# Kernel tuning notes

Measured on AMD Instinct MI355X. Metric: run time of the kernel, lower is better.

## Reference

```python
import jax, jax.numpy as jnp
import numpy as np

B, T, META = 2, 1024, 6
VOCAB, MVOCAB = 32000, 1000
D, H, L = 512, 8, 6
HS = D // H          # 64
T1 = T + META        # 1030
CHUNK = 6            # sliding/chunk granularity hard-coded in generate_matrix
LN_EPS = 1e-5


def _layernorm(x, g, b):
    mu = jnp.mean(x, axis=-1, keepdims=True)
    var = jnp.mean((x - mu) ** 2, axis=-1, keepdims=True)
    return (x - mu) * jax.lax.rsqrt(var + LN_EPS) * g + b


def _pos_encoding(t, d):
    # torch: sin((position // 6) * div_term), cos(...) interleaved even/odd
    pos = jnp.floor(jnp.arange(t, dtype=jnp.float32) / CHUNK)
    div = jnp.exp(jnp.arange(0, d, 2, dtype=jnp.float32) * (-np.log(10000.0) / d))
    ang = pos[:, None] * div[None, :]                     # [t, d/2]
    enc = jnp.zeros((t, d), dtype=jnp.float32)
    enc = enc.at[:, 0::2].set(jnp.sin(ang))
    enc = enc.at[:, 1::2].set(jnp.cos(ang))
    return enc


def _mask(n):
    # row i attends to cols [0, (i//6+1)*6) plus the last 6 (metadata) cols
    r = jnp.arange(n)
    return (r[None, :] < (r[:, None] // CHUNK + 1) * CHUNK) | (r[None, :] >= n - CHUNK)


def setup_inputs() -> dict:
    key = jax.random.key(0)
    ks = jax.random.split(key, 16)
    s = 0.02
    n = lambda k, shp: jax.random.normal(k, shp, dtype=jnp.float32) * s
    return {
        "idx": jax.random.randint(ks[0], (B, T), 0, VOCAB),
        "metadata_idx": jax.random.randint(ks[1], (B, META), 0, MVOCAB),
        "tok_emb": n(ks[2], (VOCAB, D)),
        "meta_emb": n(ks[3], (MVOCAB, D)),
        "Wq": n(ks[4], (L, H, D, HS)),
        "Wk": n(ks[5], (L, H, D, HS)),
        "Wv": n(ks[6], (L, H, D, HS)),
        "Wo": n(ks[7], (L, D, D)),
        "bo": jnp.zeros((L, D), jnp.float32),
        "W1": n(ks[8], (L, D, 4 * D)),
        "b1": jnp.zeros((L, 4 * D), jnp.float32),
        "W2": n(ks[9], (L, 4 * D, D)),
        "b2": jnp.zeros((L, D), jnp.float32),
        "ln1_g": jnp.ones((L, D), jnp.float32),
        "ln1_b": jnp.zeros((L, D), jnp.float32),
        "ln2_g": jnp.ones((L, D), jnp.float32),
        "ln2_b": jnp.zeros((L, D), jnp.float32),
        "lnf_g": jnp.ones((D,), jnp.float32),
        "lnf_b": jnp.zeros((D,), jnp.float32),
        "Wlm": n(ks[10], (D, VOCAB)),
        "blm": jnp.zeros((VOCAB,), jnp.float32),
    }


def reference(idx, metadata_idx, tok_emb, meta_emb, Wq, Wk, Wv, Wo, bo,
              W1, b1, W2, b2, ln1_g, ln1_b, ln2_g, ln2_b, lnf_g, lnf_b, Wlm, blm):
    x = tok_emb[idx] + _pos_encoding(T, D)                 # [B, T, D]
    x = jnp.concatenate([x, meta_emb[metadata_idx]], axis=1)  # [B, T1, D]
    scale = D ** -0.5          # NOTE: original scales by full n_embd, not head_size
    mask = _mask(T1)
    neg_inf = jnp.float32(-jnp.inf)
    for l in range(L):
        h = _layernorm(x, ln1_g[l], ln1_b[l])
        q = jnp.einsum('btd,hde->bhte', h, Wq[l])          # [B, H, T1, HS]
        k = jnp.einsum('btd,hde->bhte', h, Wk[l])
        v = jnp.einsum('btd,hde->bhte', h, Wv[l])
        wei = jnp.einsum('bhqe,bhke->bhqk', q, k) * scale  # [B, H, T1, T1]
        wei = jnp.where(mask, wei, neg_inf)
        wei = jax.nn.softmax(wei, axis=-1)
        o = jnp.einsum('bhqk,bhke->bhqe', wei, v)          # [B, H, T1, HS]
        o = jnp.transpose(o, (0, 2, 1, 3)).reshape(x.shape[0], T1, D)
        x = x + o @ Wo[l] + bo[l]
        h = _layernorm(x, ln2_g[l], ln2_b[l])
        x = x + jax.nn.relu(h @ W1[l] + b1[l]) @ W2[l] + b2[l]
    x = _layernorm(x, lnf_g, lnf_b)
    logits = x @ Wlm + blm                                  # [B, T1, VOCAB]
    return logits[:, :T, :]
```

## Files before the change

kernel.cpp:

```cpp
#include <hip/hip_runtime.h>
#include <hip/hip_bf16.h>
#include <math.h>

#define TT     1024
#define METAN  6
#define TT1    1030
#define BB     2
#define DD     512
#define HH     8
#define HSZ    64
#define LL     6
#define NVOCAB 32000
#define MROWS  2060
#define MPAD   2176
#define SCALE  0.044194173824159216f

typedef float  f32x4  __attribute__((ext_vector_type(4)));
typedef __bf16 bf16x8 __attribute__((ext_vector_type(8)));

__device__ __forceinline__ __bf16 f2bf(float f) { return (__bf16)f; }

__device__ __forceinline__ void glds16(const __bf16* g, const __bf16* l) {
  __builtin_amdgcn_global_load_lds(
      (const __attribute__((address_space(1))) unsigned int*)g,
      (__attribute__((address_space(3))) unsigned int*)l, 16, 0, 0);
}

__device__ __forceinline__ bf16x8 ln8v(float4 v0, float4 v1, float mu, float rs,
                                       float4 g0, float4 g1, float4 b0, float4 b1) {
  float vv[8] = {v0.x, v0.y, v0.z, v0.w, v1.x, v1.y, v1.z, v1.w};
  float gg[8] = {g0.x, g0.y, g0.z, g0.w, g1.x, g1.y, g1.z, g1.w};
  float bb[8] = {b0.x, b0.y, b0.z, b0.w, b1.x, b1.y, b1.z, b1.w};
  bf16x8 r;
#pragma unroll
  for (int j = 0; j < 8; j++) r[j] = f2bf((vv[j] - mu) * rs * gg[j] + bb[j]);
  return r;
}
__device__ __forceinline__ bf16x8 ln8(const float* xp, float mu, float rs,
                                      const float* g, const float* b) {
  return ln8v(*(const float4*)xp, *(const float4*)(xp + 4), mu, rs,
              *(const float4*)g, *(const float4*)(g + 4),
              *(const float4*)b, *(const float4*)(b + 4));
}

__global__ void k_embedw(const int* idx, const int* midx, const float* tok,
                         const float* met, float* x, float* ps, float* pq)
{
  const int sub = threadIdx.x >> 7;
  const int tl  = threadIdx.x & 127;
  const int d0  = tl * 4;
  int row = blockIdx.x * 2 + sub;
  int b = row / TT1, tk = row - b * TT1;
  float v[4];
  if (tk < TT) {
    const float* e = tok + (size_t)idx[b * TT + tk] * DD;
    float pos = (float)(tk / 6);
#pragma unroll
    for (int j = 0; j < 4; j += 2) {
      int i = (d0 + j) >> 1;
      float dv = expf((float)i * (-2.0f * 9.210340371976184f / 512.0f));
      float ang = pos * dv;
      v[j]     = e[d0 + j]     + sinf(ang);
      v[j + 1] = e[d0 + j + 1] + cosf(ang);
    }
  } else {
    const float* e = met + (size_t)midx[b * METAN + (tk - TT)] * DD;
#pragma unroll
    for (int j = 0; j < 4; j++) v[j] = e[d0 + j];
  }
  *(float4*)&x[(size_t)row * DD + d0] = *(float4*)v;
  float s = v[0] + v[1] + v[2] + v[3];
  float q = v[0]*v[0] + v[1]*v[1] + v[2]*v[2] + v[3]*v[3];
#pragma unroll
  for (int msk = 1; msk < 16; msk <<= 1) { s += __shfl_xor(s, msk); q += __shfl_xor(q, msk); }
  if ((tl & 15) == 0) {
    ps[(size_t)row * 8 + (tl >> 4)] = s;
    pq[(size_t)row * 8 + (tl >> 4)] = q;
  }
}

__global__ void k_lnpw(const float* x, const float* ps, const float* pq,
                       const float* g, const float* b, __bf16* xf)
{
  const int sub = threadIdx.x >> 6;
  const int lane = threadIdx.x & 63;
  int row = blockIdx.x * 4 + sub;
  int sr = (row >> 10) * TT1 + (row & 1023);
  float s = 0.f, q = 0.f;
#pragma unroll
  for (int j = 0; j < 8; j++) { s += ps[(size_t)sr * 8 + j]; q += pq[(size_t)sr * 8 + j]; }
  float mu = s * (1.0f / 512.0f);
  float rs = rsqrtf(fmaxf(q * (1.0f / 512.0f) - mu * mu, 0.f) + 1e-5f);
  bf16x8 o = ln8(&x[(size_t)sr * DD + lane * 8], mu, rs, &g[lane * 8], &b[lane * 8]);
  *(bf16x8*)&xf[(size_t)row * DD + lane * 8] = o;
}

__global__ void k_tcvt7(const float* __restrict__ Wq, const float* __restrict__ Wk,
                        const float* __restrict__ Wv, const float* __restrict__ Wo,
                        const float* __restrict__ W1, const float* __restrict__ W2,
                        const float* __restrict__ Wlm,
                        __bf16* __restrict__ wqkvb, __bf16* __restrict__ wob,
                        __bf16* __restrict__ w1b, __bf16* __restrict__ w2b,
                        __bf16* __restrict__ wlmb)
{
  __shared__ float t[32][33];
  int bid = blockIdx.x;
  const float* in; __bf16* out;
  int gx, gy, C, R, lo_cnt, local;
  long long in_bs, bs_hi, bs_lo;
  if (bid < 4608) {
    int job = bid / 1536; local = bid - job * 1536;
    in = job == 0 ? Wq : (job == 1 ? Wk : Wv);
    out = wqkvb + (size_t)job * 262144;
    gx = 2; gy = 16; R = 512; C = 64; in_bs = 32768; bs_hi = 786432; bs_lo = 32768; lo_cnt = 8;
  } else if (bid < 6144) {
    local = bid - 4608; in = Wo; out = wob;
    gx = 16; gy = 16; R = 512; C = 512; in_bs = 262144; bs_hi = 262144; bs_lo = 0; lo_cnt = 1;
  } else if (bid < 12288) {
    local = bid - 6144; in = W1; out = w1b;
    gx = 64; gy = 16; R = 512; C = 2048; in_bs = 1048576; bs_hi = 1048576; bs_lo = 0; lo_cnt = 1;
  } else if (bid < 18432) {
    local = bid - 12288; in = W2; out = w2b;
    gx = 16; gy = 64; R = 2048; C = 512; in_bs = 1048576; bs_hi = 1048576; bs_lo = 0; lo_cnt = 1;
  } else {
    local = bid - 18432; in = Wlm; out = wlmb;
    gx = 1000; gy = 16; R = 512; C = 32000; in_bs = 0; bs_hi = 0; bs_lo = 0; lo_cnt = 1;
  }
  int bx = local % gx; int tmp = local / gx; int by = tmp % gy; int bz = tmp / gy;
  const float* ib = in + (long long)bz * in_bs;
  __bf16* ob = out + (long long)(bz / lo_cnt) * bs_hi + (long long)(bz % lo_cnt) * bs_lo;
  int tx = threadIdx.x & 31, ty = threadIdx.x >> 5;
  int c = bx * 32 + tx;
  for (int j = ty; j < 32; j += 8)
    t[j][tx] = ib[(size_t)(by * 32 + j) * C + c];
  __syncthreads();
  int r = by * 32 + tx;
  for (int j = ty; j < 32; j += 8)
    ob[(size_t)(bx * 32 + j) * R + r] = f2bf(t[tx][j]);
}

template <int MODE, bool RELU, bool BIAS, int AMODE, int MT, int NT, int WM, bool STAT>
__device__ __forceinline__ void gemm_tiles(
    unsigned char* smem,
    const __bf16* A, const float* Ax,
    const float* ps, const float* pq,
    const float* lng, const float* lnb,
    const __bf16* __restrict__ Bt, const float* bias,
    const float* res,
    float* outf, __bf16* outb,
    float* ops, float* opq,
    int M, int N, int K, int ntx, int nty)
{
  constexpr int WN  = 4 / WM;
  constexpr int WMS = MT / WM;
  constexpr int WNS = NT / WN;
  constexpr int MR  = WMS / 16;
  constexpr int NR  = WNS / 16;
  constexpr int RA  = MT / 32;
  constexpr int RB  = NT / 32;

  __bf16* const Asm = (__bf16*)smem;
  __bf16* const Bsm = (__bf16*)smem + 2 * MT * 64;

  const int tid = threadIdx.x;
  const int lane = tid & 63, w = tid >> 6;
  const int wm = (WN == 1) ? w : (w >> 1);
  const int wn = (WN == 1) ? 0 : (w & 1);
  const int rm = lane & 15, g4 = lane >> 4;
  const int nt = ntx * nty;

  int flat = blockIdx.x;
  { const int q = nt >> 3, rr = nt & 7; const int xcd = flat & 7, ii = flat >> 3;
    flat = (xcd < rr ? xcd * (q + 1) : rr * (q + 1) + (xcd - rr) * q) + ii; }
  const int row0 = (flat % ntx) * MT;
  const int col0 = (flat / ntx) * NT;

  f32x4 acc[MR][NR];
  const f32x4 fz = {0.f, 0.f, 0.f, 0.f};
#pragma unroll
  for (int i = 0; i < MR; i++)
#pragma unroll
    for (int j = 0; j < NR; j++) acc[i][j] = fz;

  const __bf16* bSrc[RB];
#pragma unroll
  for (int i = 0; i < RB; i++) {
    int c = i * 256 + tid; int r = c >> 3; int j = (c & 7) ^ (r & 7);
    bSrc[i] = Bt + (size_t)(col0 + r) * K + j * 8;
  }
  const __bf16* aSrc[RA];
  const float *Ax0 = nullptr, *gk = nullptr, *bk = nullptr;
  float mu0 = 0.f, rs0 = 0.f;
  int oA0 = 0, oA1 = 0;
  if (AMODE == 0) {
#pragma unroll
    for (int i = 0; i < RA; i++) {
      int c = i * 256 + tid; int r = c >> 3; int j = (c & 7) ^ (r & 7);
      aSrc[i] = A + (size_t)(row0 + r) * K + j * 8;
    }
  } else {
    int srow = tid >> 2, skc = tid & 3;
    int sa0 = row0 + srow;
    Ax0 = Ax + (size_t)sa0 * DD + skc * 8;
    float s0 = 0.f, q0 = 0.f;
#pragma unroll
    for (int j = 0; j < 8; j++) { s0 += ps[(size_t)sa0 * 8 + j]; q0 += pq[(size_t)sa0 * 8 + j]; }
    mu0 = s0 * (1.0f / 512.0f);
    rs0 = rsqrtf(fmaxf(q0 * (1.0f / 512.0f) - mu0 * mu0, 0.f) + 1e-5f);
    gk = lng + skc * 8; bk = lnb + skc * 8;
    oA0 = (srow * 8 + (skc ^ (srow & 7))) * 8;
    oA1 = (srow * 8 + ((skc + 4) ^ (srow & 7))) * 8;
  }

  float4 xa0, xa1, xb0, xb1, ga0, ga1, gb0, gb1, ca0, ca1, cb0, cb1;
  auto loadA1 = [&](int k0) {
    xa0 = *(const float4*)(Ax0 + k0);      xa1 = *(const float4*)(Ax0 + k0 + 4);
    xb0 = *(const float4*)(Ax0 + k0 + 32); xb1 = *(const float4*)(Ax0 + k0 + 36);
    ga0 = *(const float4*)(gk + k0);       ga1 = *(const float4*)(gk + k0 + 4);
    gb0 = *(const float4*)(gk + k0 + 32);  gb1 = *(const float4*)(gk + k0 + 36);
    ca0 = *(const float4*)(bk + k0);       ca1 = *(const float4*)(bk + k0 + 4);
    cb0 = *(const float4*)(bk + k0 + 32);  cb1 = *(const float4*)(bk + k0 + 36);
  };
  auto writeA1 = [&](int buf) {
    *(bf16x8*)(Asm + buf * MT * 64 + oA0) = ln8v(xa0, xa1, mu0, rs0, ga0, ga1, ca0, ca1);
    *(bf16x8*)(Asm + buf * MT * 64 + oA1) = ln8v(xb0, xb1, mu0, rs0, gb0, gb1, cb0, cb1);
  };
  auto stageB = [&](int buf, int k0) {
#pragma unroll
    for (int i = 0; i < RB; i++)
      glds16(bSrc[i] + k0, Bsm + buf * NT * 64 + (i * 256 + w * 64) * 8);
  };
  auto stageA0 = [&](int buf, int k0) {
#pragma unroll
    for (int i = 0; i < RA; i++)
      glds16(aSrc[i] + k0, Asm + buf * MT * 64 + (i * 256 + w * 64) * 8);
  };

  stageB(0, 0);
  if (AMODE == 0) stageA0(0, 0);
  else { loadA1(0); writeA1(0); }
  __syncthreads();

  int cur = 0;
  for (int k0 = 0; k0 < K; k0 += 64) {
    const bool nxt = (k0 + 64 < K);
    if (nxt) {
      stageB(cur ^ 1, k0 + 64);
      if (AMODE == 0) stageA0(cur ^ 1, k0 + 64);
      else loadA1(k0 + 64);
    }
    const __bf16* Acur = Asm + cur * MT * 64;
    const __bf16* Bcur = Bsm + cur * NT * 64;
    bf16x8 af[MR][2], bf[NR][2];
#pragma unroll
    for (int m = 0; m < MR; m++) {
      int r = wm * WMS + m * 16 + rm;
      int c0 = r * 8 + (g4 ^ (r & 7));
      af[m][0] = *(const bf16x8*)(Acur + c0 * 8);
      af[m][1] = *(const bf16x8*)(Acur + (c0 ^ 4) * 8);
    }
#pragma unroll
    for (int n = 0; n < NR; n++) {
      int r = wn * WNS + n * 16 + rm;
      int c0 = r * 8 + (g4 ^ (r & 7));
      bf[n][0] = *(const bf16x8*)(Bcur + c0 * 8);
      bf[n][1] = *(const bf16x8*)(Bcur + (c0 ^ 4) * 8);
    }
#pragma unroll
    for (int t = 0; t < 2; t++)
#pragma unroll
      for (int m = 0; m < MR; m++)
#pragma unroll
        for (int n = 0; n < NR; n++)
          acc[m][n] = __builtin_amdgcn_mfma_f32_16x16x32_bf16(af[m][t], bf[n][t], acc[m][n], 0, 0, 0);
    if (nxt) {
      if (AMODE == 1) writeA1(cur ^ 1);
      __syncthreads();
    }
    cur ^= 1;
  }

  if (MODE == 2) {
    __syncthreads();
    float* T = (float*)smem;
    const int wbase = w * (32 * 68);
    const int cg = lane & 15;
#pragma unroll
    for (int h = 0; h < MR / 2; h++) {
#pragma unroll
      for (int mm = 0; mm < 2; mm++) {
        int m = h * 2 + mm;
#pragma unroll
        for (int n = 0; n < NR; n++) {
          float bvv = BIAS ? bias[col0 + wn * WNS + n * 16 + rm] : 0.f;
#pragma unroll
          for (int r = 0; r < 4; r++)
            T[wbase + (mm * 16 + g4 * 4 + r) * 68 + n * 16 + rm] = acc[m][n][r] + bvv;
        }
      }
#pragma unroll
      for (int i = 0; i < 8; i++) {
        int rloc = g4 + i * 4;
        float4 v = *(float4*)&T[wbase + rloc * 68 + cg * 4];
        *(float4*)&outf[(size_t)(row0 + wm * WMS + h * 32 + rloc) * N + col0 + wn * WNS + cg * 4] = v;
      }
    }
  } else {
#pragma unroll
    for (int m = 0; m < MR; m++) {
      int row_b = row0 + wm * WMS + m * 16 + g4 * 4;
      float bv[NR];
#pragma unroll
      for (int n = 0; n < NR; n++) bv[n] = BIAS ? bias[col0 + wn * WNS + n * 16 + rm] : 0.f;
#pragma unroll
      for (int r = 0; r < 4; r++) {
        int row = row_b + r;
        float s = 0.f, qq = 0.f;
#pragma unroll
        for (int n = 0; n < NR; n++) {
          int col = col0 + wn * WNS + n * 16 + rm;
          float v = acc[m][n][r] + bv[n];
          if (MODE == 0) {
            if (RELU) v = fmaxf(v, 0.f);
            if (row < M) outb[(size_t)row * N + col] = f2bf(v);
          } else {
            if (row < M) { v += res[(size_t)row * N + col]; outf[(size_t)row * N + col] = v; }
            s += v; qq += v * v;
          }
        }
        if (MODE == 1 && STAT) {
#pragma unroll
          for (int msk = 1; msk < 16; msk <<= 1) { s += __shfl_xor(s, msk); qq += __shfl_xor(qq, msk); }
          if (rm == 0 && row < M) {
            ops[(size_t)row * 8 + (col0 >> 6)] = s;
            opq[(size_t)row * 8 + (col0 >> 6)] = qq;
          }
        }
      }
    }
  }
}

template <int MODE, bool RELU, bool BIAS, int AMODE, int MT, int NT, int WM, bool STAT>
__global__ __launch_bounds__(256, 3) void k_gemm(
    const __bf16* A, const float* Ax, const float* ps, const float* pq,
    const float* lng, const float* lnb,
    const __bf16* __restrict__ Bt, const float* bias, const float* res,
    float* outf, __bf16* outb, float* ops, float* opq,
    int M, int N, int K, int ntx, int nty)
{
  __shared__ __align__(16) unsigned char smem[(MT + NT) * 256];
  gemm_tiles<MODE, RELU, BIAS, AMODE, MT, NT, WM, STAT>(
      smem, A, Ax, ps, pq, lng, lnb, Bt, bias, res, outf, outb, ops, opq,
      M, N, K, ntx, nty);
}

template <int MODE, bool RELU, bool BIAS, int AMODE, int MT, int NT, int WM, bool STAT>
__global__ __launch_bounds__(256, 2) void k_gemmL(
    const __bf16* A, const float* Ax, const float* ps, const float* pq,
    const float* lng, const float* lnb,
    const __bf16* __restrict__ Bt, const float* bias, const float* res,
    float* outf, __bf16* outb, float* ops, float* opq,
    int M, int N, int K, int ntx, int nty)
{
  __shared__ __align__(16) unsigned char smem[(MT + NT) * 256];
  gemm_tiles<MODE, RELU, BIAS, AMODE, MT, NT, WM, STAT>(
      smem, A, Ax, ps, pq, lng, lnb, Bt, bias, res, outf, outb, ops, opq,
      M, N, K, ntx, nty);
}

__global__ __launch_bounds__(256) void k_attnw(const __bf16* qkv, __bf16* ob)
{
  __shared__ __align__(16) __bf16 Ks[64][72];
  __shared__ __align__(16) __bf16 Vs[64][72];
  __shared__ __align__(16) __bf16 Ps[4][16][72];

  const int tid = threadIdx.x;
  const int lane = tid & 63, w = tid >> 6;
  const int rm = lane & 15, g4 = lane >> 4;
  const int skey = tid >> 3;
  const int shs = (tid & 7) * 8;
  const size_t rsd = 1536;
  const f32x4 fz = {0.f, 0.f, 0.f, 0.f};

  const int t = blockIdx.x;
  const int b = t / 136; int rem = t - b * 136;
  const int h = rem / 17;
  const int q0 = (rem % 17) * 64;
  const int qw = q0 + w * 16;

  const __bf16* qb = qkv + (size_t)b * TT1 * rsd + h * HSZ;
  const __bf16* kb = qb + 512;
  const __bf16* vb = qb + 1024;

  bf16x8 aq[2];
  {
    const __bf16* qp = qb + (size_t)(qw + rm) * rsd + 8 * g4;
    aq[0] = *(const bf16x8*)qp;
    aq[1] = *(const bf16x8*)(qp + 32);
  }

  int ae_[4];
#pragma unroll
  for (int r = 0; r < 4; r++) {
    int qr = qw + g4 * 4 + r;
    ae_[r] = (qr / 6 + 1) * 6;
  }

  float m_[4], l_[4];
  f32x4 accO[4];
#pragma unroll
  for (int j = 0; j < 4; j++) accO[j] = fz;
#pragma unroll
  for (int r = 0; r < 4; r++) { m_[r] = -1e30f; l_[r] = 0.f; }

  int aemax = ((q0 + 63) / 6 + 1) * 6;
  if (aemax > TT) aemax = TT;
  const int ntile = (aemax + 63) >> 6;

  for (int tt = 0; tt <= ntile; ++tt) {
    const bool meta = (tt == ntile);
    const int kt = meta ? TT : tt * 64;

    bf16x8 k0 = *(const bf16x8*)(kb + (size_t)(kt + skey) * rsd + shs);
    bf16x8 k1 = *(const bf16x8*)(kb + (size_t)(kt + skey + 32) * rsd + shs);
    bf16x8 v0 = *(const bf16x8*)(vb + (size_t)(kt + skey) * rsd + shs);
    bf16x8 v1 = *(const bf16x8*)(vb + (size_t)(kt + skey + 32) * rsd + shs);
    __syncthreads();
    *(bf16x8*)&Ks[skey][shs]      = k0;
    *(bf16x8*)&Ks[skey + 32][shs] = k1;
#pragma unroll
    for (int j = 0; j < 8; j++) {
      Vs[shs + j][skey]      = v0[j];
      Vs[shs + j][skey + 32] = v1[j];
    }
    __syncthreads();

    f32x4 s[4];
#pragma unroll
    for (int nt2 = 0; nt2 < 4; nt2++) {
      f32x4 a = fz;
      bf16x8 bk0 = *(const bf16x8*)&Ks[nt2 * 16 + rm][8 * g4];
      bf16x8 bk1 = *(const bf16x8*)&Ks[nt2 * 16 + rm][32 + 8 * g4];
      a = __builtin_amdgcn_mfma_f32_16x16x32_bf16(aq[0], bk0, a, 0, 0, 0);
      a = __builtin_amdgcn_mfma_f32_16x16x32_bf16(aq[1], bk1, a, 0, 0, 0);
      s[nt2] = a;
    }

    float alpha[4];
#pragma unroll
    for (int r = 0; r < 4; r++) {
      int lim = meta ? TT1 : ae_[r];
      float sv[4];
#pragma unroll
      for (int i = 0; i < 4; i++) {
        sv[i] = s[i][r] * SCALE;
        if (kt + i * 16 + rm >= lim) sv[i] = -1e30f;
      }
      float tm = fmaxf(fmaxf(sv[0], sv[1]), fmaxf(sv[2], sv[3]));
#pragma unroll
      for (int msk = 1; msk < 16; msk <<= 1) tm = fmaxf(tm, __shfl_xor(tm, msk));
      float mn = fmaxf(m_[r], tm);
      float pp[4]; float ts = 0.f;
#pragma unroll
      for (int i = 0; i < 4; i++) { pp[i] = __expf(sv[i] - mn); ts += pp[i]; }
#pragma unroll
      for (int msk = 1; msk < 16; msk <<= 1) ts += __shfl_xor(ts, msk);
      alpha[r] = __expf(m_[r] - mn);
      l_[r] = l_[r] * alpha[r] + ts;
      m_[r] = mn;
#pragma unroll
      for (int i = 0; i < 4; i++) Ps[w][g4 * 4 + r][rm + i * 16] = f2bf(pp[i]);
    }
#pragma unroll
    for (int j = 0; j < 4; j++)
#pragma unroll
      for (int r = 0; r < 4; r++) accO[j][r] *= alpha[r];
    __syncthreads();

    bf16x8 pa0 = *(const bf16x8*)&Ps[w][rm][8 * g4];
    bf16x8 pa1 = *(const bf16x8*)&Ps[w][rm][32 + 8 * g4];
#pragma unroll
    for (int j = 0; j < 4; j++) {
      bf16x8 bv0 = *(const bf16x8*)&Vs[j * 16 + rm][8 * g4];
      bf16x8 bv1 = *(const bf16x8*)&Vs[j * 16 + rm][32 + 8 * g4];
      accO[j] = __builtin_amdgcn_mfma_f32_16x16x32_bf16(pa0, bv0, accO[j], 0, 0, 0);
      accO[j] = __builtin_amdgcn_mfma_f32_16x16x32_bf16(pa1, bv1, accO[j], 0, 0, 0);
    }
  }

#pragma unroll
  for (int r = 0; r < 4; r++) {
    int q = qw + g4 * 4 + r;
    if (q < TT1) {
      float rl = 1.0f / l_[r];
#pragma unroll
      for (int j = 0; j < 4; j++)
        ob[((size_t)b * TT1 + q) * DD + h * HSZ + j * 16 + rm] = f2bf(accO[j][r] * rl);
    }
  }
}

extern "C" void kernel_launch(void* const* d_in, const int* in_sizes, int n_in,
                              void* d_out, int out_size, void* d_ws, size_t ws_size,
                              hipStream_t stream)
{
  const int*   idx   = (const int*)d_in[0];
  const int*   midx  = (const int*)d_in[1];
  const float* tok   = (const float*)d_in[2];
  const float* metae = (const float*)d_in[3];
  const float* Wq    = (const float*)d_in[4];
  const float* Wk    = (const float*)d_in[5];
  const float* Wv    = (const float*)d_in[6];
  const float* Wo    = (const float*)d_in[7];
  const float* bo    = (const float*)d_in[8];
  const float* W1    = (const float*)d_in[9];
  const float* b1    = (const float*)d_in[10];
  const float* W2    = (const float*)d_in[11];
  const float* b2    = (const float*)d_in[12];
  const float* ln1g  = (const float*)d_in[13];
  const float* ln1b  = (const float*)d_in[14];
  const float* ln2g  = (const float*)d_in[15];
  const float* ln2b  = (const float*)d_in[16];
  const float* lnfg  = (const float*)d_in[17];
  const float* lnfb  = (const float*)d_in[18];
  const float* Wlm   = (const float*)d_in[19];
  const float* blm   = (const float*)d_in[20];
  float* out = (float*)d_out;

  char* p = (char*)d_ws;
  auto alloc = [&](size_t bytes) { void* r = (void*)p; p += (bytes + 255) & ~(size_t)255; return r; };
  float*  x     = (float*)alloc((size_t)MPAD * 512 * 4);
  float*  ps_   = (float*)alloc((size_t)MPAD * 8 * 4);
  float*  pq_   = (float*)alloc((size_t)MPAD * 8 * 4);
  __bf16* qkv   = (__bf16*)alloc((size_t)MPAD * 1536 * 2);
  __bf16* obuf  = (__bf16*)alloc((size_t)MPAD * 512 * 2);
  __bf16* f1    = (__bf16*)alloc((size_t)MPAD * 2048 * 2);
  __bf16* xf    = (__bf16*)alloc((size_t)2048 * 512 * 2);
  __bf16* wqkvb = (__bf16*)alloc((size_t)6 * 1536 * 512 * 2);
  __bf16* wob   = (__bf16*)alloc((size_t)6 * 512 * 512 * 2);
  __bf16* w1b   = (__bf16*)alloc((size_t)6 * 2048 * 512 * 2);
  __bf16* w2b   = (__bf16*)alloc((size_t)6 * 512 * 2048 * 2);
  __bf16* wlmb  = (__bf16*)alloc((size_t)NVOCAB * 512 * 2);
  (void)in_sizes; (void)n_in; (void)out_size; (void)ws_size;

  k_tcvt7<<<dim3(34432), 256, 0, stream>>>(Wq, Wk, Wv, Wo, W1, W2, Wlm,
                                           wqkvb, wob, w1b, w2b, wlmb);

  k_embedw<<<dim3(1030), 256, 0, stream>>>(idx, midx, tok, metae, x, ps_, pq_);

  for (int l = 0; l < LL; ++l) {
    k_gemm<0, false, false, 1, 64, 64, 4, false><<<dim3(816), 256, 0, stream>>>(
        nullptr, x, ps_, pq_, ln1g + l * 512, ln1b + l * 512,
        wqkvb + (size_t)l * 786432, nullptr, nullptr, nullptr, qkv,
        nullptr, nullptr, MROWS, 1536, 512, 34, 24);
    k_attnw<<<dim3(272), 256, 0, stream>>>(qkv, obuf);
    k_gemm<1, false, true, 0, 64, 64, 4, true><<<dim3(272), 256, 0, stream>>>(
        obuf, nullptr, nullptr, nullptr, nullptr, nullptr,
        wob + (size_t)l * 262144, bo + l * 512, x, x, nullptr,
        ps_, pq_, MROWS, 512, 512, 34, 8);
    k_gemm<0, true, true, 1, 64, 64, 4, false><<<dim3(1088), 256, 0, stream>>>(
        nullptr, x, ps_, pq_, ln2g + l * 512, ln2b + l * 512,
        w1b + (size_t)l * 1048576, b1 + l * 2048, nullptr, nullptr, f1,
        nullptr, nullptr, MROWS, 2048, 512, 34, 32);
    k_gemm<1, false, true, 0, 64, 64, 4, true><<<dim3(272), 256, 0, stream>>>(
        f1, nullptr, nullptr, nullptr, nullptr, nullptr,
        w2b + (size_t)l * 1048576, b2 + l * 512, x, x, nullptr,
        ps_, pq_, MROWS, 512, 2048, 34, 8);
  }

  k_lnpw<<<dim3(512), 256, 0, stream>>>(x, ps_, pq_, lnfg, lnfb, xf);
  k_gemmL<2, false, true, 0, 128, 128, 2, false><<<dim3(4000), 256, 0, stream>>>(
      xf, nullptr, nullptr, nullptr, nullptr, nullptr,
      wlmb, blm, nullptr, out, nullptr, nullptr, nullptr, 2048, NVOCAB, 512, 16, 250);
}
```

Before: 979.3 us.

## Fuse embedding into weight-convert kernel, deepen K-step for residual GEMMs, add MFMA priority

```diff
diff --git a/kernel.cpp b/kernel.cpp
--- a/kernel.cpp
+++ b/kernel.cpp
@@ -43,42 +43,6 @@
               *(const float4*)b, *(const float4*)(b + 4));
 }
 
-__global__ void k_embedw(const int* idx, const int* midx, const float* tok,
-                         const float* met, float* x, float* ps, float* pq)
-{
-  const int sub = threadIdx.x >> 7;
-  const int tl  = threadIdx.x & 127;
-  const int d0  = tl * 4;
-  int row = blockIdx.x * 2 + sub;
-  int b = row / TT1, tk = row - b * TT1;
-  float v[4];
-  if (tk < TT) {
-    const float* e = tok + (size_t)idx[b * TT + tk] * DD;
-    float pos = (float)(tk / 6);
-#pragma unroll
-    for (int j = 0; j < 4; j += 2) {
-      int i = (d0 + j) >> 1;
-      float dv = expf((float)i * (-2.0f * 9.210340371976184f / 512.0f));
-      float ang = pos * dv;
-      v[j]     = e[d0 + j]     + sinf(ang);
-      v[j + 1] = e[d0 + j + 1] + cosf(ang);
-    }
-  } else {
-    const float* e = met + (size_t)midx[b * METAN + (tk - TT)] * DD;
-#pragma unroll
-    for (int j = 0; j < 4; j++) v[j] = e[d0 + j];
-  }
-  *(float4*)&x[(size_t)row * DD + d0] = *(float4*)v;
-  float s = v[0] + v[1] + v[2] + v[3];
-  float q = v[0]*v[0] + v[1]*v[1] + v[2]*v[2] + v[3]*v[3];
-#pragma unroll
-  for (int msk = 1; msk < 16; msk <<= 1) { s += __shfl_xor(s, msk); q += __shfl_xor(q, msk); }
-  if ((tl & 15) == 0) {
-    ps[(size_t)row * 8 + (tl >> 4)] = s;
-    pq[(size_t)row * 8 + (tl >> 4)] = q;
-  }
-}
-
 __global__ void k_lnpw(const float* x, const float* ps, const float* pq,
                        const float* g, const float* b, __bf16* xf)
 {
@@ -95,16 +59,52 @@
   *(bf16x8*)&xf[(size_t)row * DD + lane * 8] = o;
 }
 
-__global__ void k_tcvt7(const float* __restrict__ Wq, const float* __restrict__ Wk,
+__global__ void k_tcvt8(const float* __restrict__ Wq, const float* __restrict__ Wk,
                         const float* __restrict__ Wv, const float* __restrict__ Wo,
                         const float* __restrict__ W1, const float* __restrict__ W2,
                         const float* __restrict__ Wlm,
                         __bf16* __restrict__ wqkvb, __bf16* __restrict__ wob,
                         __bf16* __restrict__ w1b, __bf16* __restrict__ w2b,
-                        __bf16* __restrict__ wlmb)
-{
+                        __bf16* __restrict__ wlmb,
+                        const int* idx, const int* midx, const float* tok,
+                        const float* met, float* x, float* ps, float* pq)
+{
+  int bid = blockIdx.x;
+  if (bid >= 34432) {
+    const int sub = threadIdx.x >> 7;
+    const int tl  = threadIdx.x & 127;
+    const int d0  = tl * 4;
+    int row = (bid - 34432) * 2 + sub;
+    int b = row / TT1, tk = row - b * TT1;
+    float v[4];
+    if (tk < TT) {
+      const float* e = tok + (size_t)idx[b * TT + tk] * DD;
+      float pos = (float)(tk / 6);
+#pragma unroll
+      for (int j = 0; j < 4; j += 2) {
+        int i = (d0 + j) >> 1;
+        float dv = expf((float)i * (-2.0f * 9.210340371976184f / 512.0f));
+        float ang = pos * dv;
+        v[j]     = e[d0 + j]     + sinf(ang);
+        v[j + 1] = e[d0 + j + 1] + cosf(ang);
+      }
+    } else {
+      const float* e = met + (size_t)midx[b * METAN + (tk - TT)] * DD;
+#pragma unroll
+      for (int j = 0; j < 4; j++) v[j] = e[d0 + j];
+    }
+    *(float4*)&x[(size_t)row * DD + d0] = *(float4*)v;
+    float s = v[0] + v[1] + v[2] + v[3];
+    float q = v[0]*v[0] + v[1]*v[1] + v[2]*v[2] + v[3]*v[3];
+#pragma unroll
+    for (int msk = 1; msk < 16; msk <<= 1) { s += __shfl_xor(s, msk); q += __shfl_xor(q, msk); }
+    if ((tl & 15) == 0) {
+      ps[(size_t)row * 8 + (tl >> 4)] = s;
+      pq[(size_t)row * 8 + (tl >> 4)] = q;
+    }
+    return;
+  }
   __shared__ float t[32][33];
-  int bid = blockIdx.x;
   const float* in; __bf16* out;
   int gx, gy, C, R, lo_cnt, local;
   long long in_bs, bs_hi, bs_lo;
@@ -139,7 +139,7 @@
     ob[(size_t)(bx * 32 + j) * R + r] = f2bf(t[tx][j]);
 }
 
-template <int MODE, bool RELU, bool BIAS, int AMODE, int MT, int NT, int WM, bool STAT>
+template <int MODE, bool RELU, bool BIAS, int AMODE, int MT, int NT, int WM, bool STAT, int KS>
 __device__ __forceinline__ void gemm_tiles(
     unsigned char* smem,
     const __bf16* A, const float* Ax,
@@ -160,7 +160,7 @@
   constexpr int RB  = NT / 32;
 
   __bf16* const Asm = (__bf16*)smem;
-  __bf16* const Bsm = (__bf16*)smem + 2 * MT * 64;
+  __bf16* const Bsm = (__bf16*)smem + 2 * KS * MT * 64;
 
   const int tid = threadIdx.x;
   const int lane = tid & 63, w = tid >> 6;
@@ -222,18 +222,22 @@
     cb0 = *(const float4*)(bk + k0 + 32);  cb1 = *(const float4*)(bk + k0 + 36);
   };
   auto writeA1 = [&](int buf) {
-    *(bf16x8*)(Asm + buf * MT * 64 + oA0) = ln8v(xa0, xa1, mu0, rs0, ga0, ga1, ca0, ca1);
-    *(bf16x8*)(Asm + buf * MT * 64 + oA1) = ln8v(xb0, xb1, mu0, rs0, gb0, gb1, cb0, cb1);
+    *(bf16x8*)(Asm + buf * KS * MT * 64 + oA0) = ln8v(xa0, xa1, mu0, rs0, ga0, ga1, ca0, ca1);
+    *(bf16x8*)(Asm + buf * KS * MT * 64 + oA1) = ln8v(xb0, xb1, mu0, rs0, gb0, gb1, cb0, cb1);
   };
   auto stageB = [&](int buf, int k0) {
 #pragma unroll
-    for (int i = 0; i < RB; i++)
-      glds16(bSrc[i] + k0, Bsm + buf * NT * 64 + (i * 256 + w * 64) * 8);
+    for (int h = 0; h < KS; h++)
+#pragma unroll
+      for (int i = 0; i < RB; i++)
+        glds16(bSrc[i] + k0 + h * 64, Bsm + (buf * KS + h) * NT * 64 + (i * 256 + w * 64) * 8);
   };
   auto stageA0 = [&](int buf, int k0) {
 #pragma unroll
-    for (int i = 0; i < RA; i++)
-      glds16(aSrc[i] + k0, Asm + buf * MT * 64 + (i * 256 + w * 64) * 8);
+    for (int h = 0; h < KS; h++)
+#pragma unroll
+      for (int i = 0; i < RA; i++)
+        glds16(aSrc[i] + k0 + h * 64, Asm + (buf * KS + h) * MT * 64 + (i * 256 + w * 64) * 8);
   };
 
   stageB(0, 0);
@@ -242,37 +246,41 @@
   __syncthreads();
 
   int cur = 0;
-  for (int k0 = 0; k0 < K; k0 += 64) {
-    const bool nxt = (k0 + 64 < K);
+  const int BK = 64 * KS;
+  for (int k0 = 0; k0 < K; k0 += BK) {
+    const bool nxt = (k0 + BK < K);
     if (nxt) {
-      stageB(cur ^ 1, k0 + 64);
-      if (AMODE == 0) stageA0(cur ^ 1, k0 + 64);
-      else loadA1(k0 + 64);
-    }
-    const __bf16* Acur = Asm + cur * MT * 64;
-    const __bf16* Bcur = Bsm + cur * NT * 64;
-    bf16x8 af[MR][2], bf[NR][2];
-#pragma unroll
-    for (int m = 0; m < MR; m++) {
-      int r = wm * WMS + m * 16 + rm;
-      int c0 = r * 8 + (g4 ^ (r & 7));
-      af[m][0] = *(const bf16x8*)(Acur + c0 * 8);
-      af[m][1] = *(const bf16x8*)(Acur + (c0 ^ 4) * 8);
-    }
-#pragma unroll
-    for (int n = 0; n < NR; n++) {
-      int r = wn * WNS + n * 16 + rm;
-      int c0 = r * 8 + (g4 ^ (r & 7));
-      bf[n][0] = *(const bf16x8*)(Bcur + c0 * 8);
-      bf[n][1] = *(const bf16x8*)(Bcur + (c0 ^ 4) * 8);
-    }
-#pragma unroll
-    for (int t = 0; t < 2; t++)
-#pragma unroll
-      for (int m = 0; m < MR; m++)
-#pragma unroll
-        for (int n = 0; n < NR; n++)
-          acc[m][n] = __builtin_amdgcn_mfma_f32_16x16x32_bf16(af[m][t], bf[n][t], acc[m][n], 0, 0, 0);
+      stageB(cur ^ 1, k0 + BK);
+      if (AMODE == 0) stageA0(cur ^ 1, k0 + BK);
+      else loadA1(k0 + BK);
+    }
+#pragma unroll
+    for (int h = 0; h < KS; h++) {
+      const __bf16* Acur = Asm + (cur * KS + h) * MT * 64;
+      const __bf16* Bcur = Bsm + (cur * KS + h) * NT * 64;
+      bf16x8 af[MR][2], bf[NR][2];
+#pragma unroll
+      for (int m = 0; m < MR; m++) {
+        int r = wm * WMS + m * 16 + rm;
+        int c0 = r * 8 + (g4 ^ (r & 7));
+        af[m][0] = *(const bf16x8*)(Acur + c0 * 8);
+        af[m][1] = *(const bf16x8*)(Acur + (c0 ^ 4) * 8);
+      }
+#pragma unroll
+      for (int n = 0; n < NR; n++) {
+        int r = wn * WNS + n * 16 + rm;
+        int c0 = r * 8 + (g4 ^ (r & 7));
+        bf[n][0] = *(const bf16x8*)(Bcur + c0 * 8);
+        bf[n][1] = *(const bf16x8*)(Bcur + (c0 ^ 4) * 8);
+      }
+#pragma unroll
+      for (int t = 0; t < 2; t++)
+#pragma unroll
+        for (int m = 0; m < MR; m++)
+#pragma unroll
+          for (int n = 0; n < NR; n++)
+            acc[m][n] = __builtin_amdgcn_mfma_f32_16x16x32_bf16(af[m][t], bf[n][t], acc[m][n], 0, 0, 0);
+    }
     if (nxt) {
       if (AMODE == 1) writeA1(cur ^ 1);
       __syncthreads();
@@ -350,7 +358,21 @@
     int M, int N, int K, int ntx, int nty)
 {
   __shared__ __align__(16) unsigned char smem[(MT + NT) * 256];
-  gemm_tiles<MODE, RELU, BIAS, AMODE, MT, NT, WM, STAT>(
+  gemm_tiles<MODE, RELU, BIAS, AMODE, MT, NT, WM, STAT, 1>(
+      smem, A, Ax, ps, pq, lng, lnb, Bt, bias, res, outf, outb, ops, opq,
+      M, N, K, ntx, nty);
+}
+
+template <int MODE, bool RELU, bool BIAS, int MT, int NT, int WM, bool STAT>
+__global__ __launch_bounds__(256, 2) void k_gemm2(
+    const __bf16* A, const float* Ax, const float* ps, const float* pq,
+    const float* lng, const float* lnb,
+    const __bf16* __restrict__ Bt, const float* bias, const float* res,
+    float* outf, __bf16* outb, float* ops, float* opq,
+    int M, int N, int K, int ntx, int nty)
+{
+  __shared__ __align__(16) unsigned char smem[(MT + NT) * 512];
+  gemm_tiles<MODE, RELU, BIAS, 0, MT, NT, WM, STAT, 2>(
       smem, A, Ax, ps, pq, lng, lnb, Bt, bias, res, outf, outb, ops, opq,
       M, N, K, ntx, nty);
 }
@@ -364,7 +386,7 @@
     int M, int N, int K, int ntx, int nty)
 {
   __shared__ __align__(16) unsigned char smem[(MT + NT) * 256];
-  gemm_tiles<MODE, RELU, BIAS, AMODE, MT, NT, WM, STAT>(
+  gemm_tiles<MODE, RELU, BIAS, AMODE, MT, NT, WM, STAT, 1>(
       smem, A, Ax, ps, pq, lng, lnb, Bt, bias, res, outf, outb, ops, opq,
       M, N, K, ntx, nty);
 }
@@ -437,6 +459,7 @@
     __syncthreads();
 
     f32x4 s[4];
+    __builtin_amdgcn_s_setprio(1);
 #pragma unroll
     for (int nt2 = 0; nt2 < 4; nt2++) {
       f32x4 a = fz;
@@ -446,6 +469,7 @@
       a = __builtin_amdgcn_mfma_f32_16x16x32_bf16(aq[1], bk1, a, 0, 0, 0);
       s[nt2] = a;
     }
+    __builtin_amdgcn_s_setprio(0);
 
     float alpha[4];
 #pragma unroll
@@ -480,6 +504,7 @@
 
     bf16x8 pa0 = *(const bf16x8*)&Ps[w][rm][8 * g4];
     bf16x8 pa1 = *(const bf16x8*)&Ps[w][rm][32 + 8 * g4];
+    __builtin_amdgcn_s_setprio(1);
 #pragma unroll
     for (int j = 0; j < 4; j++) {
       bf16x8 bv0 = *(const bf16x8*)&Vs[j * 16 + rm][8 * g4];
@@ -487,6 +512,7 @@
       accO[j] = __builtin_amdgcn_mfma_f32_16x16x32_bf16(pa0, bv0, accO[j], 0, 0, 0);
       accO[j] = __builtin_amdgcn_mfma_f32_16x16x32_bf16(pa1, bv1, accO[j], 0, 0, 0);
     }
+    __builtin_amdgcn_s_setprio(0);
   }
 
 #pragma unroll
@@ -544,10 +570,9 @@
   __bf16* wlmb  = (__bf16*)alloc((size_t)NVOCAB * 512 * 2);
   (void)in_sizes; (void)n_in; (void)out_size; (void)ws_size;
 
-  k_tcvt7<<<dim3(34432), 256, 0, stream>>>(Wq, Wk, Wv, Wo, W1, W2, Wlm,
-                                           wqkvb, wob, w1b, w2b, wlmb);
-
-  k_embedw<<<dim3(1030), 256, 0, stream>>>(idx, midx, tok, metae, x, ps_, pq_);
+  k_tcvt8<<<dim3(35462), 256, 0, stream>>>(Wq, Wk, Wv, Wo, W1, W2, Wlm,
+                                           wqkvb, wob, w1b, w2b, wlmb,
+                                           idx, midx, tok, metae, x, ps_, pq_);
 
   for (int l = 0; l < LL; ++l) {
     k_gemm<0, false, false, 1, 64, 64, 4, false><<<dim3(816), 256, 0, stream>>>(
@@ -555,7 +580,7 @@
         wqkvb + (size_t)l * 786432, nullptr, nullptr, nullptr, qkv,
         nullptr, nullptr, MROWS, 1536, 512, 34, 24);
     k_attnw<<<dim3(272), 256, 0, stream>>>(qkv, obuf);
-    k_gemm<1, false, true, 0, 64, 64, 4, true><<<dim3(272), 256, 0, stream>>>(
+    k_gemm2<1, false, true, 64, 64, 4, true><<<dim3(272), 256, 0, stream>>>(
         obuf, nullptr, nullptr, nullptr, nullptr, nullptr,
         wob + (size_t)l * 262144, bo + l * 512, x, x, nullptr,
         ps_, pq_, MROWS, 512, 512, 34, 8);
@@ -563,7 +588,7 @@
         nullptr, x, ps_, pq_, ln2g + l * 512, ln2b + l * 512,
         w1b + (size_t)l * 1048576, b1 + l * 2048, nullptr, nullptr, f1,
         nullptr, nullptr, MROWS, 2048, 512, 34, 32);
-    k_gemm<1, false, true, 0, 64, 64, 4, true><<<dim3(272), 256, 0, stream>>>(
+    k_gemm2<1, false, true, 64, 64, 4, true><<<dim3(272), 256, 0, stream>>>(
         f1, nullptr, nullptr, nullptr, nullptr, nullptr,
         w2b + (size_t)l * 1048576, b2 + l * 512, x, x, nullptr,
         ps_, pq_, MROWS, 512, 2048, 34, 8);
```

New measurement: 940.4 us. -4.0%, faster.
